# Kernel tuning notes

Hardware: AMD Instinct MI355X
Metric: run time of the kernel (lower is better)

The kernel has to match this reference:

```python
import jax, jax.numpy as jnp
import numpy as np

K = 3          # kernel_size
STRIDE = 1
PAD = 1
DIL = 1


def setup_inputs() -> dict:
    key = jax.random.key(0)
    k1, k2, k3, k4, k5 = jax.random.split(key, 5)
    x = jax.random.normal(k1, (4, 64, 128, 128), jnp.float32)
    weight = jax.random.normal(k2, (64, 64, K, K), jnp.float32) * 0.05   # [O, C, K, K]
    bias = jax.random.normal(k3, (64,), jnp.float32) * 0.05
    # offset conv params: small nonzero so offsets actually exercise bilinear sampling
    offset_w = jax.random.normal(k4, (2 * K * K, 64, K, K), jnp.float32) * 0.01
    offset_b = jax.random.normal(k5, (2 * K * K,), jnp.float32) * 0.1
    return {"x": x, "weight": weight, "bias": bias,
            "offset_w": offset_w, "offset_b": offset_b}


def _conv2d(x, w, b):
    y = jax.lax.conv_general_dilated(
        x, w, window_strides=(STRIDE, STRIDE),
        padding=((PAD, PAD), (PAD, PAD)), rhs_dilation=(DIL, DIL),
        dimension_numbers=("NCHW", "OIHW", "NCHW"))
    return y + b[None, :, None, None]


def _bilinear_sample(img, ys, xs):
    # img: [C, H, W]; ys, xs: [KK, Ho, Wo] float sampling coords
    H, W = img.shape[1], img.shape[2]
    y0 = jnp.floor(ys)
    x0 = jnp.floor(xs)
    y1 = y0 + 1.0
    x1 = x0 + 1.0
    wy1 = ys - y0
    wx1 = xs - x0
    wy0 = 1.0 - wy1
    wx0 = 1.0 - wx1

    def gather(yy, xx):
        valid = (yy >= 0) & (yy <= H - 1) & (xx >= 0) & (xx <= W - 1)
        yi = jnp.clip(yy, 0, H - 1).astype(jnp.int32)
        xi = jnp.clip(xx, 0, W - 1).astype(jnp.int32)
        v = img[:, yi, xi]                     # [C, KK, Ho, Wo]
        return v * valid.astype(img.dtype)

    return (gather(y0, x0) * (wy0 * wx0) + gather(y0, x1) * (wy0 * wx1)
            + gather(y1, x0) * (wy1 * wx0) + gather(y1, x1) * (wy1 * wx1))


def reference(x, weight, bias, offset_w, offset_b):
    B, C, H, W = x.shape
    KK = K * K
    # offsets: [B, 2*K*K, Ho, Wo], per-location (dy, dx) for each kernel tap
    offset = _conv2d(x, offset_w, offset_b)
    Ho, Wo = offset.shape[2], offset.shape[3]
    off = offset.reshape(B, KK, 2, Ho, Wo)
    dy, dx = off[:, :, 0], off[:, :, 1]        # [B, KK, Ho, Wo]

    ki, kj = jnp.meshgrid(jnp.arange(K), jnp.arange(K), indexing="ij")
    ki = ki.reshape(KK).astype(x.dtype)
    kj = kj.reshape(KK).astype(x.dtype)
    oy = (jnp.arange(Ho) * STRIDE - PAD).astype(x.dtype)
    ox = (jnp.arange(Wo) * STRIDE - PAD).astype(x.dtype)
    base_y = oy[None, :, None] + (ki * DIL)[:, None, None]   # [KK, Ho, 1]
    base_x = ox[None, None, :] + (kj * DIL)[:, None, None]   # [KK, 1, Wo]
    ys = base_y[None] + dy                                   # [B, KK, Ho, Wo]
    xs = base_x[None] + dx

    # sampled: [B, C, KK, Ho, Wo]
    sampled = jax.vmap(_bilinear_sample)(x, ys, xs)
    w = weight.reshape(weight.shape[0], C, KK)
    out = jnp.einsum("bckhw,ock->bohw", sampled, w) + bias[None, :, None, None]
    return out
```

## Files before the change

kernel.cpp:

```cpp
#include <hip/hip_runtime.h>
#include <hip/hip_bf16.h>

#define B_ 4
#define C_ 64
#define H_ 128
#define W_ 128
#define HW_ (H_ * W_)
#define OCH_ 18

typedef __attribute__((ext_vector_type(8))) short short8;
typedef __attribute__((ext_vector_type(16))) float f32x16;

#define W2B_ELEMS (9 * 2 * 4 * 64 * 8)
#define W2A_ELEMS (36 * 64 * 8)
#define OFF_BYTE_OFS 131072
#define XH_BYTE_OFS  2490368
#define WS_NEED (XH_BYTE_OFS + (size_t)B_ * H_ * W_ * C_ * 2)

#define PSTRIDE_B 10256
#define WIN_BYTES (4 * PSTRIDE_B)

__device__ __forceinline__ unsigned short f2bf(float f) {
  union { float f; unsigned u; } v; v.f = f;
  unsigned r = v.u + 0x7FFFu + ((v.u >> 16) & 1u);
  return (unsigned short)(r >> 16);
}
__device__ __forceinline__ float bf2f(unsigned short h) {
  union { unsigned u; float f; } v; v.u = ((unsigned)h) << 16;
  return v.f;
}
__device__ __forceinline__ short f2bfh(float f) {
  __hip_bfloat16 h = __float2bfloat16(f);
  return *reinterpret_cast<short*>(&h);
}
__device__ __forceinline__ int swz512(int x) { return (x & 7) * 64 + (x >> 3); }

__device__ __forceinline__ void pack_weights_body(
    int idx, const float* __restrict__ wmain, const float* __restrict__ offw,
    unsigned short* __restrict__ ws_u) {
  if (idx < W2B_ELEMS) {
    int i = idx & 7, lane = (idx >> 3) & 63, s = (idx >> 9) & 3;
    int mq = (idx >> 11) & 1, t = idx >> 12;
    int o = mq * 32 + (lane & 31);
    int c = 16 * s + (lane >> 5) * 8 + i;
    ws_u[idx] = f2bf(wmain[(o * 64 + c) * 9 + t]);
  } else if (idx < W2B_ELEMS + W2A_ELEMS) {
    int j = idx - W2B_ELEMS;
    int i = j & 7, lane = (j >> 3) & 63, s = j >> 9;
    int kg = 16 * s + (lane >> 5) * 8 + i;
    int t = kg >> 6, c = kg & 63, oc = lane & 31;
    ws_u[idx] = (oc < OCH_) ? f2bf(offw[(oc * 64 + c) * 9 + t]) : (unsigned short)0;
  }
}

__global__ __launch_bounds__(256) void prep_kernel(
    const float* __restrict__ x, const float* __restrict__ wmain,
    const float* __restrict__ offw, unsigned short* __restrict__ ws_u,
    unsigned short* __restrict__ xh) {
  const int tid = threadIdx.x;
  if (blockIdx.x < 512) {
    __shared__ float s[W_ * 65];
    const int h = blockIdx.x & (H_ - 1);
    const int b = blockIdx.x >> 7;
    const float* xb = x + ((size_t)b * C_ * H_ + h) * W_;
    for (int i = tid; i < C_ * W_; i += 256) {
      int c = i >> 7, w = i & (W_ - 1);
      s[w * 65 + c] = xb[(size_t)c * HW_ + w];
    }
    __syncthreads();
    unsigned short* dst = xh + ((size_t)(b * H_ + h) * W_) * C_;
    for (int i = tid; i < W_ * 8; i += 256) {
      int w = i >> 3, g = i & 7;
      short8 v;
      #pragma unroll
      for (int j = 0; j < 8; ++j) v[j] = (short)f2bf(s[w * 65 + g * 8 + j]);
      *(short8*)&dst[w * C_ + g * 8] = v;
    }
  } else {
    pack_weights_body((blockIdx.x - 512) * 256 + tid, wmain, offw, ws_u);
  }
}

__global__ __launch_bounds__(256) void pack_w_only(
    const float* __restrict__ wmain, const float* __restrict__ offw,
    unsigned short* __restrict__ ws_u) {
  pack_weights_body(blockIdx.x * 256 + threadIdx.x, wmain, offw, ws_u);
}

template<int KI, int KJ, int CPH>
__device__ __forceinline__ void tap_body(
    float dy, float dx, int ho, int px, int lane, int b,
    const char* __restrict__ win, const unsigned short* __restrict__ xh,
    const unsigned short* __restrict__ wt2,
    f32x16& acc0, f32x16& acc1) {
  const float ys = (float)(ho - 1 + KI) + dy;
  const float xs = (float)(px - 1 + KJ) + dx;
  const float y0f = floorf(ys), x0f = floorf(xs);
  const int y0 = (int)y0f, x0 = (int)x0f;
  const int y1 = y0 + 1, x1 = x0 + 1;
  const float wy1 = ys - y0f, wx1 = xs - x0f;
  const float wy0 = 1.f - wy1, wx0 = 1.f - wx1;
  const bool vy0 = (unsigned)y0 < (unsigned)H_, vy1 = (unsigned)y1 < (unsigned)H_;
  const bool vx0 = (unsigned)x0 < (unsigned)W_, vx1 = (unsigned)x1 < (unsigned)W_;
  const float g00 = (vy0 && vx0) ? wy0 * wx0 : 0.f;
  const float g01 = (vy0 && vx1) ? wy0 * wx1 : 0.f;
  const float g10 = (vy1 && vx0) ? wy1 * wx0 : 0.f;
  const float g11 = (vy1 && vx1) ? wy1 * wx1 : 0.f;
  const int yc0 = min(max(y0, 0), H_ - 1), yc1 = min(max(y1, 0), H_ - 1);
  const int xc0 = min(max(x0, 0), W_ - 1), xc1 = min(max(x1, 0), W_ - 1);
  const int rr0 = yc0 - ho + 2, rr1 = yc1 - ho + 2;
  const bool in0 = (unsigned)rr0 < 5u, in1 = (unsigned)rr1 < 5u;
  const int r0 = min(max(rr0, 0), 4), r1 = min(max(rr1, 0), 4);
  const int u00 = (r0 * 128 + xc0) << 4, u01 = (r0 * 128 + xc1) << 4;
  const int u10 = (r1 * 128 + xc0) << 4, u11 = (r1 * 128 + xc1) << 4;
  const int laneh = lane >> 5;
  #pragma unroll
  for (int ssl = 0; ssl < 2; ++ssl) {
    const int ss = CPH * 2 + ssl;
    const char* pb = win + (2 * ssl + laneh) * PSTRIDE_B;
    short8 c00 = *(const short8*)(pb + u00);
    short8 c01 = *(const short8*)(pb + u01);
    short8 c10 = *(const short8*)(pb + u10);
    short8 c11 = *(const short8*)(pb + u11);
    if (!in0 || !in1) {
      const int ch8 = (2 * ss + laneh) << 3;
      if (!in0) {
        c00 = *(const short8*)&xh[(((size_t)((b * H_ + yc0) * W_ + xc0)) << 6) + ch8];
        c01 = *(const short8*)&xh[(((size_t)((b * H_ + yc0) * W_ + xc1)) << 6) + ch8];
      }
      if (!in1) {
        c10 = *(const short8*)&xh[(((size_t)((b * H_ + yc1) * W_ + xc0)) << 6) + ch8];
        c11 = *(const short8*)&xh[(((size_t)((b * H_ + yc1) * W_ + xc1)) << 6) + ch8];
      }
    }
    short8 bf;
    #pragma unroll
    for (int i = 0; i < 8; ++i) {
      float v = g00 * bf2f((unsigned short)c00[i]) + g01 * bf2f((unsigned short)c01[i])
              + g10 * bf2f((unsigned short)c10[i]) + g11 * bf2f((unsigned short)c11[i]);
      bf[i] = f2bfh(v);
    }
    const short8 a0 = *(const short8*)&wt2[(ss * 64 + lane) * 8];
    const short8 a1 = *(const short8*)&wt2[((4 + ss) * 64 + lane) * 8];
    acc0 = __builtin_amdgcn_mfma_f32_32x32x16_bf16(a0, bf, acc0, 0, 0, 0);
    acc1 = __builtin_amdgcn_mfma_f32_32x32x16_bf16(a1, bf, acc1, 0, 0, 0);
  }
}

#define STAGEW(CPH)                                                                     \
  _Pragma("unroll")                                                                     \
  for (int it = 0; it < 5; ++it) {                                                      \
    const int i = tid + it * 512;                                                       \
    const int p = i & 3;                                                                \
    const int xcol = (i >> 2) & 127;                                                    \
    const int r = i >> 9;                                                               \
    const int srow = min(H_ - 1, max(0, ho - 2 + r));                                   \
    const short8 v = *(const short8*)&xh[(((size_t)((b * H_ + srow) * W_ + xcol)) << 6) \
                                         + ((4 * (CPH) + p) << 3)];                     \
    *(short8*)(smem + p * PSTRIDE_B + ((r * 128 + xcol) << 4)) = v;                     \
  }

#define P1HALF(CPH)                                                                     \
  _Pragma("unroll")                                                                     \
  for (int t = 0; t < 9; ++t) {                                                         \
    _Pragma("unroll")                                                                   \
    for (int q = 0; q < 2; ++q) {                                                       \
      const int s = 4 * t + 2 * (CPH) + q;                                              \
      const int ki = t / 3, kj = t - 3 * (t / 3);                                       \
      const int row = ho - 1 + ki, col = px - 1 + kj;                                   \
      short8 bfr = {0, 0, 0, 0, 0, 0, 0, 0};                                            \
      if (((unsigned)row < (unsigned)H_) && ((unsigned)col < (unsigned)W_))             \
        bfr = *(const short8*)(smem + (2 * q + laneh) * PSTRIDE_B                       \
                               + (((ki + 1) * 128 + col) << 4));                        \
      const short8 afr = *(const short8*)&w2a[((size_t)s * 64 + lane) * 8];             \
      pacc = __builtin_amdgcn_mfma_f32_32x32x16_bf16(afr, bfr, pacc, 0, 0, 0);          \
    }                                                                                   \
  }

#define EXT(T, J)                                                                       \
  {                                                                                     \
    constexpr int ocy = 2 * (T), ocx = 2 * (T) + 1;                                     \
    constexpr int ry = (ocy & 3) + 4 * (ocy >> 3), hy = (ocy >> 2) & 1;                 \
    constexpr int rx = (ocx & 3) + 4 * (ocx >> 3), hx = (ocx >> 2) & 1;                 \
    dys[J] = __shfl(pacc[ry], (lane & 31) + (hy << 5)) + ob[ocy];                       \
    dxs[J] = __shfl(pacc[rx], (lane & 31) + (hx << 5)) + ob[ocx];                       \
  }

#define TAP(KI, KJ, CPH, J)                                                             \
  tap_body<KI, KJ, CPH>(dys[J], dxs[J], ho, px, lane, b, smem, xh,                      \
                        w2b + ((KI) * 3 + (KJ)) * 4096, acc0, acc1)

#define P2CPH(CPH)                                                                      \
  if (sub == 0) {                                                                       \
    TAP(0, 0, CPH, 0); TAP(0, 1, CPH, 1); TAP(0, 2, CPH, 2); TAP(1, 0, CPH, 3);         \
  } else {                                                                              \
    TAP(1, 1, CPH, 0); TAP(1, 2, CPH, 1); TAP(2, 0, CPH, 2); TAP(2, 1, CPH, 3);         \
    TAP(2, 2, CPH, 4);                                                                  \
  }

__global__ __launch_bounds__(512, 4) void deform_fused2(
    const unsigned short* __restrict__ xh, const float* __restrict__ bias,
    const float* __restrict__ ob, const unsigned short* __restrict__ w2b,
    const unsigned short* __restrict__ w2a, float* __restrict__ out) {
  const int blk = swz512(blockIdx.x);
  const int ho = blk & (H_ - 1);
  const int b  = blk >> 7;
  const int tid = threadIdx.x;
  const int lane = tid & 63;
  const int wave = tid >> 6;
  const int pair = wave >> 1;
  const int sub  = wave & 1;
  const int px   = pair * 32 + (lane & 31);
  const int laneh = lane >> 5;

  __shared__ __align__(16) char smem[WIN_BYTES];

  f32x16 pacc;
  #pragma unroll
  for (int r = 0; r < 16; ++r) pacc[r] = 0.f;

  STAGEW(0);
  __syncthreads();
  P1HALF(0);
  __syncthreads();
  STAGEW(1);
  __syncthreads();
  P1HALF(1);

  float dys[5], dxs[5];
  if (sub == 0) {
    EXT(0, 0); EXT(1, 1); EXT(2, 2); EXT(3, 3);
    dys[4] = 0.f; dxs[4] = 0.f;
  } else {
    EXT(4, 0); EXT(5, 1); EXT(6, 2); EXT(7, 3); EXT(8, 4);
  }

  f32x16 acc0, acc1;
  #pragma unroll
  for (int r = 0; r < 16; ++r) { acc0[r] = 0.f; acc1[r] = 0.f; }

  P2CPH(1);
  __syncthreads();
  STAGEW(0);
  __syncthreads();
  P2CPH(0);
  __syncthreads();

  float* red = (float*)smem;
  if (sub) {
    #pragma unroll
    for (int i = 0; i < 16; ++i) {
      red[(i * 4 + pair) * 64 + lane]        = acc0[i];
      red[((16 + i) * 4 + pair) * 64 + lane] = acc1[i];
    }
  }
  __syncthreads();
  if (!sub) {
    #pragma unroll
    for (int i = 0; i < 16; ++i) {
      acc0[i] += red[(i * 4 + pair) * 64 + lane];
      acc1[i] += red[((16 + i) * 4 + pair) * 64 + lane];
    }
    #pragma unroll
    for (int reg = 0; reg < 16; ++reg) {
      int row = (reg & 3) + 8 * (reg >> 2) + 4 * laneh;
      out[((b * 64 + row)      * H_ + ho) * W_ + px] = acc0[reg] + bias[row];
      out[((b * 64 + 32 + row) * H_ + ho) * W_ + px] = acc1[reg] + bias[32 + row];
    }
  }
}

__global__ __launch_bounds__(256) void offset_conv_mfma(
    const float* __restrict__ x, const float* __restrict__ ob,
    const unsigned short* __restrict__ w2a, unsigned short* __restrict__ offout) {
  const int ho = blockIdx.x & (H_ - 1);
  const int b  = blockIdx.x >> 7;
  const int tid = threadIdx.x;
  const int lane = tid & 63;
  const int wv = tid >> 6;
  __shared__ __align__(16) unsigned short sx[3 * 130 * 64];
  const float* xb = x + (size_t)b * C_ * HW_;
  for (int i = tid; i < 96 * 130; i += 256) {
    int col = i % 130;
    int c2  = i / 130;
    int r   = c2 >> 5;
    int c   = (c2 & 31) * 2;
    int row = ho - 1 + r, gcol = col - 1;
    float v0 = 0.f, v1 = 0.f;
    if ((unsigned)row < (unsigned)H_ && (unsigned)gcol < (unsigned)W_) {
      v0 = xb[(size_t)c * HW_ + row * W_ + gcol];
      v1 = xb[(size_t)(c + 1) * HW_ + row * W_ + gcol];
    }
    unsigned pk = (unsigned)f2bf(v0) | ((unsigned)f2bf(v1) << 16);
    int cblk = (c >> 3) ^ (col & 7);
    int h = ((r * 130 + col) * 8 + cblk) * 8 + (c & 7);
    *(unsigned*)&sx[h] = pk;
  }
  __syncthreads();
  const int px  = wv * 32 + (lane & 31);
  const int cbh = lane >> 5;
  f32x16 acc;
  #pragma unroll
  for (int r = 0; r < 16; ++r) acc[r] = 0.f;
  for (int s = 0; s < 36; ++s) {
    int t  = s >> 2;
    int ki = t / 3, kj = t - 3 * ki;
    int j  = px + kj;
    int cblk = (s & 3) * 2 + cbh;
    const short8 bfr = *(const short8*)&sx[((ki * 130 + j) * 8 + (cblk ^ (j & 7))) * 8];
    const short8 afr = *(const short8*)&w2a[(s * 64 + lane) * 8];
    acc = __builtin_amdgcn_mfma_f32_32x32x16_bf16(afr, bfr, acc, 0, 0, 0);
  }
  #pragma unroll
  for (int reg = 0; reg < 16; ++reg) {
    int oc = (reg & 3) + 8 * (reg >> 2) + 4 * (lane >> 5);
    if (oc < OCH_) {
      float v = acc[reg] + ob[oc];
      offout[((b * OCH_ + oc) * H_ + ho) * W_ + px] = f2bf(v);
    }
  }
}

__global__ __launch_bounds__(256) void deform_mfma(
    const float* __restrict__ x, const float* __restrict__ bias,
    const unsigned short* __restrict__ w2b, const unsigned short* __restrict__ offb,
    float* __restrict__ out) {
  const int ho = blockIdx.x & (H_ - 1);
  const int b  = blockIdx.x >> 7;
  const int lane = threadIdx.x & 63;
  const int wv   = threadIdx.x >> 6;
  const int px   = wv * 32 + (lane & 31);
  const int cb   = (lane >> 5) * 8;
  const float* xb = x + (size_t)b * C_ * HW_;
  f32x16 acc0, acc1;
  #pragma unroll
  for (int r = 0; r < 16; ++r) { acc0[r] = 0.f; acc1[r] = 0.f; }
  for (int t = 0; t < 9; ++t) {
    const int ki = t / 3, kj = t - 3 * ki;
    float dy = bf2f(offb[((b * OCH_ + 2 * t)     * H_ + ho) * W_ + px]);
    float dx = bf2f(offb[((b * OCH_ + 2 * t + 1) * H_ + ho) * W_ + px]);
    float ys = (float)(ho - 1 + ki) + dy;
    float xs = (float)(px - 1 + kj) + dx;
    float y0f = floorf(ys), x0f = floorf(xs);
    int y0 = (int)y0f, x0 = (int)x0f;
    int y1 = y0 + 1,   x1 = x0 + 1;
    float wy1 = ys - y0f, wx1 = xs - x0f;
    float wy0 = 1.f - wy1, wx0 = 1.f - wx1;
    bool vy0 = (unsigned)y0 < (unsigned)H_, vy1 = (unsigned)y1 < (unsigned)H_;
    bool vx0 = (unsigned)x0 < (unsigned)W_, vx1 = (unsigned)x1 < (unsigned)W_;
    int yc0 = min(max(y0, 0), H_ - 1), yc1 = min(max(y1, 0), H_ - 1);
    int xc0 = min(max(x0, 0), W_ - 1), xc1 = min(max(x1, 0), W_ - 1);
    const int o00 = yc0 * W_ + xc0, o01 = yc0 * W_ + xc1;
    const int o10 = yc1 * W_ + xc0, o11 = yc1 * W_ + xc1;
    const float g00 = (vy0 && vx0) ? wy0 * wx0 : 0.f;
    const float g01 = (vy0 && vx1) ? wy0 * wx1 : 0.f;
    const float g10 = (vy1 && vx0) ? wy1 * wx0 : 0.f;
    const float g11 = (vy1 && vx1) ? wy1 * wx1 : 0.f;
    const short8* wp = (const short8*)(w2b + (size_t)t * 2 * 4 * 64 * 8);
    short8 a0[4], a1[4];
    #pragma unroll
    for (int s = 0; s < 4; ++s) {
      a0[s] = wp[s * 64 + lane];
      a1[s] = wp[(4 + s) * 64 + lane];
    }
    #pragma unroll
    for (int s = 0; s < 4; ++s) {
      const int cidx = (cb + 16 * s) * HW_;
      short8 bf;
      #pragma unroll
      for (int i = 0; i < 8; ++i) {
        const int bi = cidx + i * HW_;
        float v = g00 * xb[bi + o00] + g01 * xb[bi + o01]
                + g10 * xb[bi + o10] + g11 * xb[bi + o11];
        bf[i] = (short)f2bf(v);
      }
      acc0 = __builtin_amdgcn_mfma_f32_32x32x16_bf16(a0[s], bf, acc0, 0, 0, 0);
      acc1 = __builtin_amdgcn_mfma_f32_32x32x16_bf16(a1[s], bf, acc1, 0, 0, 0);
    }
  }
  #pragma unroll
  for (int reg = 0; reg < 16; ++reg) {
    int row = (reg & 3) + 8 * (reg >> 2) + 4 * (lane >> 5);
    out[((b * 64 + row)      * H_ + ho) * W_ + px] = acc0[reg] + bias[row];
    out[((b * 64 + 32 + row) * H_ + ho) * W_ + px] = acc1[reg] + bias[32 + row];
  }
}

extern "C" void kernel_launch(void* const* d_in, const int* in_sizes, int n_in,
                              void* d_out, int out_size, void* d_ws, size_t ws_size,
                              hipStream_t stream) {
  const float* x    = (const float*)d_in[0];
  const float* wt   = (const float*)d_in[1];
  const float* bias = (const float*)d_in[2];
  const float* ow   = (const float*)d_in[3];
  const float* ob   = (const float*)d_in[4];
  float* out = (float*)d_out;

  unsigned short* ws_u  = (unsigned short*)d_ws;
  unsigned short* w2b   = ws_u;
  unsigned short* w2a   = ws_u + W2B_ELEMS;
  unsigned short* offbf = (unsigned short*)((char*)d_ws + OFF_BYTE_OFS);
  unsigned short* xh    = (unsigned short*)((char*)d_ws + XH_BYTE_OFS);

  const int pack_blocks = (W2B_ELEMS + W2A_ELEMS + 255) / 256;

  if (ws_size >= WS_NEED) {
    prep_kernel<<<512 + pack_blocks, 256, 0, stream>>>(x, wt, ow, ws_u, xh);
    deform_fused2<<<512, 512, 0, stream>>>(xh, bias, ob, w2b, w2a, out);
  } else {
    pack_w_only<<<pack_blocks, 256, 0, stream>>>(wt, ow, ws_u);
    offset_conv_mfma<<<B_ * H_, 256, 0, stream>>>(x, ob, w2a, offbf);
    deform_mfma<<<B_ * H_, 256, 0, stream>>>(x, bias, w2b, offbf, out);
  }
}
```

Measured before the change: 43.05 us.

## Split fused deformable conv into half-row tiles with narrower LDS window

The fused kernel now processes half an output row (64 columns) per block with 256 threads instead of a full row with 512, doubling the grid to 1024 blocks. The staged LDS window shrinks to 72 columns with halo, which lowers shared memory per block and may raise occupancy. Samples falling outside the window fall back to global loads. The bilinear blend also unpacks bf16 pairs with packed float2 arithmetic. In exchange, neighbouring blocks restage overlapping halo columns, and more samples take the slower global-memory path.

Result: slower. 45.94 us (+6.7%).

```diff
diff --git a/kernel.cpp b/kernel.cpp
--- a/kernel.cpp
+++ b/kernel.cpp
@@ -10,6 +10,7 @@
 
 typedef __attribute__((ext_vector_type(8))) short short8;
 typedef __attribute__((ext_vector_type(16))) float f32x16;
+typedef __attribute__((ext_vector_type(2))) float float2v;
 
 #define W2B_ELEMS (9 * 2 * 4 * 64 * 8)
 #define W2A_ELEMS (36 * 64 * 8)
@@ -17,7 +18,8 @@
 #define XH_BYTE_OFS  2490368
 #define WS_NEED (XH_BYTE_OFS + (size_t)B_ * H_ * W_ * C_ * 2)
 
-#define PSTRIDE_B 10256
+#define WCOLS 72
+#define PSTRIDE_B (5 * WCOLS * 16 + 16)
 #define WIN_BYTES (4 * PSTRIDE_B)
 
 __device__ __forceinline__ unsigned short f2bf(float f) {
@@ -29,11 +31,15 @@
   union { unsigned u; float f; } v; v.u = ((unsigned)h) << 16;
   return v.f;
 }
-__device__ __forceinline__ short f2bfh(float f) {
+__device__ __forceinline__ unsigned short f2bfh(float f) {
   __hip_bfloat16 h = __float2bfloat16(f);
-  return *reinterpret_cast<short*>(&h);
-}
-__device__ __forceinline__ int swz512(int x) { return (x & 7) * 64 + (x >> 3); }
+  return *reinterpret_cast<unsigned short*>(&h);
+}
+__device__ __forceinline__ float uaf(unsigned u) {
+  union { unsigned u; float f; } v; v.u = u; return v.f;
+}
+__device__ __forceinline__ int swz512(int x)  { return (x & 7) * 64  + (x >> 3); }
+__device__ __forceinline__ int swz1024(int x) { return (x & 7) * 128 + (x >> 3); }
 
 __device__ __forceinline__ void pack_weights_body(
     int idx, const float* __restrict__ wmain, const float* __restrict__ offw,
@@ -89,7 +95,7 @@
 
 template<int KI, int KJ, int CPH>
 __device__ __forceinline__ void tap_body(
-    float dy, float dx, int ho, int px, int lane, int b,
+    float dy, float dx, int ho, int wo0, int px, int lane, int b,
     const char* __restrict__ win, const unsigned short* __restrict__ xh,
     const unsigned short* __restrict__ wt2,
     f32x16& acc0, f32x16& acc1) {
@@ -109,10 +115,13 @@
   const int yc0 = min(max(y0, 0), H_ - 1), yc1 = min(max(y1, 0), H_ - 1);
   const int xc0 = min(max(x0, 0), W_ - 1), xc1 = min(max(x1, 0), W_ - 1);
   const int rr0 = yc0 - ho + 2, rr1 = yc1 - ho + 2;
-  const bool in0 = (unsigned)rr0 < 5u, in1 = (unsigned)rr1 < 5u;
+  const int cc0 = xc0 - wo0 + 4, cc1 = xc1 - wo0 + 4;
+  const bool inw = ((unsigned)rr0 < 5u) & ((unsigned)rr1 < 5u) &
+                   ((unsigned)cc0 < (unsigned)WCOLS) & ((unsigned)cc1 < (unsigned)WCOLS);
   const int r0 = min(max(rr0, 0), 4), r1 = min(max(rr1, 0), 4);
-  const int u00 = (r0 * 128 + xc0) << 4, u01 = (r0 * 128 + xc1) << 4;
-  const int u10 = (r1 * 128 + xc0) << 4, u11 = (r1 * 128 + xc1) << 4;
+  const int c0 = min(max(cc0, 0), WCOLS - 1), c1 = min(max(cc1, 0), WCOLS - 1);
+  const int u00 = (r0 * WCOLS + c0) << 4, u01 = (r0 * WCOLS + c1) << 4;
+  const int u10 = (r1 * WCOLS + c0) << 4, u11 = (r1 * WCOLS + c1) << 4;
   const int laneh = lane >> 5;
   #pragma unroll
   for (int ssl = 0; ssl < 2; ++ssl) {
@@ -122,23 +131,27 @@
     short8 c01 = *(const short8*)(pb + u01);
     short8 c10 = *(const short8*)(pb + u10);
     short8 c11 = *(const short8*)(pb + u11);
-    if (!in0 || !in1) {
-      const int ch8 = (2 * ss + laneh) << 3;
-      if (!in0) {
-        c00 = *(const short8*)&xh[(((size_t)((b * H_ + yc0) * W_ + xc0)) << 6) + ch8];
-        c01 = *(const short8*)&xh[(((size_t)((b * H_ + yc0) * W_ + xc1)) << 6) + ch8];
-      }
-      if (!in1) {
-        c10 = *(const short8*)&xh[(((size_t)((b * H_ + yc1) * W_ + xc0)) << 6) + ch8];
-        c11 = *(const short8*)&xh[(((size_t)((b * H_ + yc1) * W_ + xc1)) << 6) + ch8];
-      }
+    if (!inw) {
+      const size_t ch8 = (size_t)((2 * ss + laneh) << 3);
+      c00 = *(const short8*)&xh[(((size_t)((b * H_ + yc0) * W_ + xc0)) << 6) + ch8];
+      c01 = *(const short8*)&xh[(((size_t)((b * H_ + yc0) * W_ + xc1)) << 6) + ch8];
+      c10 = *(const short8*)&xh[(((size_t)((b * H_ + yc1) * W_ + xc0)) << 6) + ch8];
+      c11 = *(const short8*)&xh[(((size_t)((b * H_ + yc1) * W_ + xc1)) << 6) + ch8];
     }
     short8 bf;
     #pragma unroll
-    for (int i = 0; i < 8; ++i) {
-      float v = g00 * bf2f((unsigned short)c00[i]) + g01 * bf2f((unsigned short)c01[i])
-              + g10 * bf2f((unsigned short)c10[i]) + g11 * bf2f((unsigned short)c11[i]);
-      bf[i] = f2bfh(v);
+    for (int d = 0; d < 4; ++d) {
+      const unsigned w00 = ((const unsigned*)&c00)[d];
+      const unsigned w01 = ((const unsigned*)&c01)[d];
+      const unsigned w10 = ((const unsigned*)&c10)[d];
+      const unsigned w11 = ((const unsigned*)&c11)[d];
+      float2v p00, p01, p10, p11;
+      p00.x = uaf(w00 << 16); p00.y = uaf(w00 & 0xFFFF0000u);
+      p01.x = uaf(w01 << 16); p01.y = uaf(w01 & 0xFFFF0000u);
+      p10.x = uaf(w10 << 16); p10.y = uaf(w10 & 0xFFFF0000u);
+      p11.x = uaf(w11 << 16); p11.y = uaf(w11 & 0xFFFF0000u);
+      float2v v = p00 * g00 + p01 * g01 + p10 * g10 + p11 * g11;
+      ((unsigned*)&bf)[d] = (unsigned)f2bfh(v.x) | ((unsigned)f2bfh(v.y) << 16);
     }
     const short8 a0 = *(const short8*)&wt2[(ss * 64 + lane) * 8];
     const short8 a1 = *(const short8*)&wt2[((4 + ss) * 64 + lane) * 8];
@@ -147,17 +160,23 @@
   }
 }
 
+#define NLOAD (4 * 5 * WCOLS)
+
 #define STAGEW(CPH)                                                                     \
   _Pragma("unroll")                                                                     \
-  for (int it = 0; it < 5; ++it) {                                                      \
-    const int i = tid + it * 512;                                                       \
-    const int p = i & 3;                                                                \
-    const int xcol = (i >> 2) & 127;                                                    \
-    const int r = i >> 9;                                                               \
-    const int srow = min(H_ - 1, max(0, ho - 2 + r));                                   \
-    const short8 v = *(const short8*)&xh[(((size_t)((b * H_ + srow) * W_ + xcol)) << 6) \
-                                         + ((4 * (CPH) + p) << 3)];                     \
-    *(short8*)(smem + p * PSTRIDE_B + ((r * 128 + xcol) << 4)) = v;                     \
+  for (int it = 0; it < 6; ++it) {                                                      \
+    const int i = tid + it * 256;                                                       \
+    if (i < NLOAD) {                                                                    \
+      const int p = i & 3;                                                              \
+      const int j = i >> 2;                                                             \
+      const int col = j % WCOLS;                                                        \
+      const int r = j / WCOLS;                                                          \
+      const int srow = min(H_ - 1, max(0, ho - 2 + r));                                 \
+      const int scol = min(W_ - 1, max(0, wo0 - 4 + col));                              \
+      const short8 v = *(const short8*)&xh[(((size_t)((b * H_ + srow) * W_ + scol)) << 6) \
+                                           + ((4 * (CPH) + p) << 3)];                   \
+      *(short8*)(smem + p * PSTRIDE_B + ((r * WCOLS + col) << 4)) = v;                  \
+    }                                                                                   \
   }
 
 #define P1HALF(CPH)                                                                     \
@@ -171,7 +190,7 @@
       short8 bfr = {0, 0, 0, 0, 0, 0, 0, 0};                                            \
       if (((unsigned)row < (unsigned)H_) && ((unsigned)col < (unsigned)W_))             \
         bfr = *(const short8*)(smem + (2 * q + laneh) * PSTRIDE_B                       \
-                               + (((ki + 1) * 128 + col) << 4));                        \
+                               + (((ki + 1) * WCOLS + (pxl + 3 + kj)) << 4));           \
       const short8 afr = *(const short8*)&w2a[((size_t)s * 64 + lane) * 8];             \
       pacc = __builtin_amdgcn_mfma_f32_32x32x16_bf16(afr, bfr, pacc, 0, 0, 0);          \
     }                                                                                   \
@@ -187,7 +206,7 @@
   }
 
 #define TAP(KI, KJ, CPH, J)                                                             \
-  tap_body<KI, KJ, CPH>(dys[J], dxs[J], ho, px, lane, b, smem, xh,                      \
+  tap_body<KI, KJ, CPH>(dys[J], dxs[J], ho, wo0, px, lane, b, smem, xh,                 \
                         w2b + ((KI) * 3 + (KJ)) * 4096, acc0, acc1)
 
 #define P2CPH(CPH)                                                                      \
@@ -198,19 +217,22 @@
     TAP(2, 2, CPH, 4);                                                                  \
   }
 
-__global__ __launch_bounds__(512, 4) void deform_fused2(
+__global__ __launch_bounds__(256, 4) void deform_fused3(
     const unsigned short* __restrict__ xh, const float* __restrict__ bias,
     const float* __restrict__ ob, const unsigned short* __restrict__ w2b,
     const unsigned short* __restrict__ w2a, float* __restrict__ out) {
-  const int blk = swz512(blockIdx.x);
-  const int ho = blk & (H_ - 1);
-  const int b  = blk >> 7;
+  const int blk = swz1024(blockIdx.x);
+  const int whalf = blk & 1;
+  const int ho = (blk >> 1) & (H_ - 1);
+  const int b  = blk >> 8;
+  const int wo0 = whalf * 64;
   const int tid = threadIdx.x;
   const int lane = tid & 63;
   const int wave = tid >> 6;
   const int pair = wave >> 1;
   const int sub  = wave & 1;
-  const int px   = pair * 32 + (lane & 31);
+  const int pxl  = pair * 32 + (lane & 31);
+  const int px   = wo0 + pxl;
   const int laneh = lane >> 5;
 
   __shared__ __align__(16) char smem[WIN_BYTES];
@@ -250,16 +272,16 @@
   if (sub) {
     #pragma unroll
     for (int i = 0; i < 16; ++i) {
-      red[(i * 4 + pair) * 64 + lane]        = acc0[i];
-      red[((16 + i) * 4 + pair) * 64 + lane] = acc1[i];
+      red[(i * 2 + pair) * 64 + lane]        = acc0[i];
+      red[((16 + i) * 2 + pair) * 64 + lane] = acc1[i];
     }
   }
   __syncthreads();
   if (!sub) {
     #pragma unroll
     for (int i = 0; i < 16; ++i) {
-      acc0[i] += red[(i * 4 + pair) * 64 + lane];
-      acc1[i] += red[((16 + i) * 4 + pair) * 64 + lane];
+      acc0[i] += red[(i * 2 + pair) * 64 + lane];
+      acc1[i] += red[((16 + i) * 2 + pair) * 64 + lane];
     }
     #pragma unroll
     for (int reg = 0; reg < 16; ++reg) {
@@ -406,7 +428,7 @@
 
   if (ws_size >= WS_NEED) {
     prep_kernel<<<512 + pack_blocks, 256, 0, stream>>>(x, wt, ow, ws_u, xh);
-    deform_fused2<<<512, 512, 0, stream>>>(xh, bias, ob, w2b, w2a, out);
+    deform_fused3<<<1024, 256, 0, stream>>>(xh, bias, ob, w2b, w2a, out);
   } else {
     pack_w_only<<<pack_blocks, 256, 0, stream>>>(wt, ow, ws_u);
     offset_conv_mfma<<<B_ * H_, 256, 0, stream>>>(x, ob, w2a, offbf);
```

## Prefetch staged windows into registers to overlap global loads with MFMA phases

Applied to the files above, without the earlier changes.

Splits the shared-memory window staging into a register-prefetch issue step and a later write step, so global loads for the next channel half (and for the phase-2 restage) are in flight while the offset-conv MFMAs run. It also splits the offset accumulator into two independent MFMA chains to break the serial dependency, and vectorises the prep kernel's transpose loads to float4. The cost is extra registers (five short8 staging values plus a second accumulator) under a 512-thread, 4-block launch bound, which may cause spills or lower occupancy.

After: 44.82 us. 4.1% more time.

```diff
diff --git a/kernel.cpp b/kernel.cpp
--- a/kernel.cpp
+++ b/kernel.cpp
@@ -63,9 +63,13 @@
     const int h = blockIdx.x & (H_ - 1);
     const int b = blockIdx.x >> 7;
     const float* xb = x + ((size_t)b * C_ * H_ + h) * W_;
-    for (int i = tid; i < C_ * W_; i += 256) {
-      int c = i >> 7, w = i & (W_ - 1);
-      s[w * 65 + c] = xb[(size_t)c * HW_ + w];
+    for (int i = tid; i < C_ * W_ / 4; i += 256) {
+      int c = i >> 5, q = i & 31;
+      float4 v = *reinterpret_cast<const float4*>(&xb[(size_t)c * HW_ + q * 4]);
+      s[(q * 4 + 0) * 65 + c] = v.x;
+      s[(q * 4 + 1) * 65 + c] = v.y;
+      s[(q * 4 + 2) * 65 + c] = v.z;
+      s[(q * 4 + 3) * 65 + c] = v.w;
     }
     __syncthreads();
     unsigned short* dst = xh + ((size_t)(b * H_ + h) * W_) * C_;
@@ -147,17 +151,28 @@
   }
 }
 
-#define STAGEW(CPH)                                                                     \
+#define STAGE_ISSUE(CPH)                                                                \
   _Pragma("unroll")                                                                     \
   for (int it = 0; it < 5; ++it) {                                                      \
     const int i = tid + it * 512;                                                       \
     const int p = i & 3;                                                                \
-    const int xcol = (i >> 2) & 127;                                                    \
-    const int r = i >> 9;                                                               \
+    const int j = i >> 2;                                                               \
+    const int col = j & 127;                                                            \
+    const int r = j >> 7;                                                               \
     const int srow = min(H_ - 1, max(0, ho - 2 + r));                                   \
-    const short8 v = *(const short8*)&xh[(((size_t)((b * H_ + srow) * W_ + xcol)) << 6) \
-                                         + ((4 * (CPH) + p) << 3)];                     \
-    *(short8*)(smem + p * PSTRIDE_B + ((r * 128 + xcol) << 4)) = v;                     \
+    stg[it] = *(const short8*)&xh[(((size_t)((b * H_ + srow) * W_ + col)) << 6)         \
+                                  + ((4 * (CPH) + p) << 3)];                            \
+  }
+
+#define STAGE_WRITE()                                                                   \
+  _Pragma("unroll")                                                                     \
+  for (int it = 0; it < 5; ++it) {                                                      \
+    const int i = tid + it * 512;                                                       \
+    const int p = i & 3;                                                                \
+    const int j = i >> 2;                                                               \
+    const int col = j & 127;                                                            \
+    const int r = j >> 7;                                                               \
+    *(short8*)(smem + p * PSTRIDE_B + ((r * 128 + col) << 4)) = stg[it];                \
   }
 
 #define P1HALF(CPH)                                                                     \
@@ -173,7 +188,10 @@
         bfr = *(const short8*)(smem + (2 * q + laneh) * PSTRIDE_B                       \
                                + (((ki + 1) * 128 + col) << 4));                        \
       const short8 afr = *(const short8*)&w2a[((size_t)s * 64 + lane) * 8];             \
-      pacc = __builtin_amdgcn_mfma_f32_32x32x16_bf16(afr, bfr, pacc, 0, 0, 0);          \
+      if (q == 0)                                                                       \
+        pacc_a = __builtin_amdgcn_mfma_f32_32x32x16_bf16(afr, bfr, pacc_a, 0, 0, 0);    \
+      else                                                                              \
+        pacc_b = __builtin_amdgcn_mfma_f32_32x32x16_bf16(afr, bfr, pacc_b, 0, 0, 0);    \
     }                                                                                   \
   }
 
@@ -198,7 +216,7 @@
     TAP(2, 2, CPH, 4);                                                                  \
   }
 
-__global__ __launch_bounds__(512, 4) void deform_fused2(
+__global__ __launch_bounds__(512, 4) void deform_fused4(
     const unsigned short* __restrict__ xh, const float* __restrict__ bias,
     const float* __restrict__ ob, const unsigned short* __restrict__ w2b,
     const unsigned short* __restrict__ w2a, float* __restrict__ out) {
@@ -215,17 +233,28 @@
 
   __shared__ __align__(16) char smem[WIN_BYTES];
 
+  short8 stg[5];
+
+  f32x16 pacc_a, pacc_b;
+  #pragma unroll
+  for (int r = 0; r < 16; ++r) { pacc_a[r] = 0.f; pacc_b[r] = 0.f; }
+
+  STAGE_ISSUE(0);
+  STAGE_WRITE();
+  __syncthreads();
+
+  STAGE_ISSUE(1);
+  P1HALF(0);
+  __syncthreads();
+  STAGE_WRITE();
+  __syncthreads();
+
+  STAGE_ISSUE(0);
+  P1HALF(1);
+
   f32x16 pacc;
   #pragma unroll
-  for (int r = 0; r < 16; ++r) pacc[r] = 0.f;
-
-  STAGEW(0);
-  __syncthreads();
-  P1HALF(0);
-  __syncthreads();
-  STAGEW(1);
-  __syncthreads();
-  P1HALF(1);
+  for (int r = 0; r < 16; ++r) pacc[r] = pacc_a[r] + pacc_b[r];
 
   float dys[5], dxs[5];
   if (sub == 0) {
@@ -241,7 +270,7 @@
 
   P2CPH(1);
   __syncthreads();
-  STAGEW(0);
+  STAGE_WRITE();
   __syncthreads();
   P2CPH(0);
   __syncthreads();
@@ -406,7 +435,7 @@
 
   if (ws_size >= WS_NEED) {
     prep_kernel<<<512 + pack_blocks, 256, 0, stream>>>(x, wt, ow, ws_u, xh);
-    deform_fused2<<<512, 512, 0, stream>>>(xh, bias, ob, w2b, w2a, out);
+    deform_fused4<<<512, 512, 0, stream>>>(xh, bias, ob, w2b, w2a, out);
   } else {
     pack_w_only<<<pack_blocks, 256, 0, stream>>>(wt, ow, ws_u);
     offset_conv_mfma<<<B_ * H_, 256, 0, stream>>>(x, ob, w2a, offbf);
```

## Stage full 64-channel window once and split offset conv across wave pairs

Applied to the files above, without the earlier changes.

The fused deformable-conv kernel now stages all 64 channels of the 5-row input window into shared memory in a single pass, using register-batched loads, instead of two half-channel passes that needed restaging and extra barriers. The offset-conv MFMA work is split between the two waves of each pair, each doing half the k-steps with two independent accumulators. Their partial sums are reduced through shared memory rather than by shuffles. The prep kernel transposes input with float4 loads. Shared memory roughly doubles and launch bounds drop to 2 blocks per CU, which may reduce occupancy.

Result: no change. 42.43 us (-1.4%).

```diff
diff --git a/kernel.cpp b/kernel.cpp
--- a/kernel.cpp
+++ b/kernel.cpp
@@ -18,7 +18,9 @@
 #define WS_NEED (XH_BYTE_OFS + (size_t)B_ * H_ * W_ * C_ * 2)
 
 #define PSTRIDE_B 10256
-#define WIN_BYTES (4 * PSTRIDE_B)
+#define WIN_BYTES (8 * PSTRIDE_B)
+#define PART_OFS  WIN_BYTES
+#define SMEM_BYTES (WIN_BYTES + 2 * 4 * 18 * 32 * 4)
 
 __device__ __forceinline__ unsigned short f2bf(float f) {
   union { float f; unsigned u; } v; v.f = f;
@@ -63,9 +65,13 @@
     const int h = blockIdx.x & (H_ - 1);
     const int b = blockIdx.x >> 7;
     const float* xb = x + ((size_t)b * C_ * H_ + h) * W_;
-    for (int i = tid; i < C_ * W_; i += 256) {
-      int c = i >> 7, w = i & (W_ - 1);
-      s[w * 65 + c] = xb[(size_t)c * HW_ + w];
+    for (int i = tid; i < C_ * W_ / 4; i += 256) {
+      int c = i >> 5, q = i & 31;
+      float4 v = *reinterpret_cast<const float4*>(&xb[(size_t)c * HW_ + q * 4]);
+      s[(q * 4 + 0) * 65 + c] = v.x;
+      s[(q * 4 + 1) * 65 + c] = v.y;
+      s[(q * 4 + 2) * 65 + c] = v.z;
+      s[(q * 4 + 3) * 65 + c] = v.w;
     }
     __syncthreads();
     unsigned short* dst = xh + ((size_t)(b * H_ + h) * W_) * C_;
@@ -87,8 +93,8 @@
   pack_weights_body(blockIdx.x * 256 + threadIdx.x, wmain, offw, ws_u);
 }
 
-template<int KI, int KJ, int CPH>
-__device__ __forceinline__ void tap_body(
+template<int KI, int KJ>
+__device__ __forceinline__ void tap_full(
     float dy, float dx, int ho, int px, int lane, int b,
     const char* __restrict__ win, const unsigned short* __restrict__ xh,
     const unsigned short* __restrict__ wt2,
@@ -115,9 +121,8 @@
   const int u10 = (r1 * 128 + xc0) << 4, u11 = (r1 * 128 + xc1) << 4;
   const int laneh = lane >> 5;
   #pragma unroll
-  for (int ssl = 0; ssl < 2; ++ssl) {
-    const int ss = CPH * 2 + ssl;
-    const char* pb = win + (2 * ssl + laneh) * PSTRIDE_B;
+  for (int ss = 0; ss < 4; ++ss) {
+    const char* pb = win + (2 * ss + laneh) * PSTRIDE_B;
     short8 c00 = *(const short8*)(pb + u00);
     short8 c01 = *(const short8*)(pb + u01);
     short8 c10 = *(const short8*)(pb + u10);
@@ -147,58 +152,11 @@
   }
 }
 
-#define STAGEW(CPH)                                                                     \
-  _Pragma("unroll")                                                                     \
-  for (int it = 0; it < 5; ++it) {                                                      \
-    const int i = tid + it * 512;                                                       \
-    const int p = i & 3;                                                                \
-    const int xcol = (i >> 2) & 127;                                                    \
-    const int r = i >> 9;                                                               \
-    const int srow = min(H_ - 1, max(0, ho - 2 + r));                                   \
-    const short8 v = *(const short8*)&xh[(((size_t)((b * H_ + srow) * W_ + xcol)) << 6) \
-                                         + ((4 * (CPH) + p) << 3)];                     \
-    *(short8*)(smem + p * PSTRIDE_B + ((r * 128 + xcol) << 4)) = v;                     \
-  }
-
-#define P1HALF(CPH)                                                                     \
-  _Pragma("unroll")                                                                     \
-  for (int t = 0; t < 9; ++t) {                                                         \
-    _Pragma("unroll")                                                                   \
-    for (int q = 0; q < 2; ++q) {                                                       \
-      const int s = 4 * t + 2 * (CPH) + q;                                              \
-      const int ki = t / 3, kj = t - 3 * (t / 3);                                       \
-      const int row = ho - 1 + ki, col = px - 1 + kj;                                   \
-      short8 bfr = {0, 0, 0, 0, 0, 0, 0, 0};                                            \
-      if (((unsigned)row < (unsigned)H_) && ((unsigned)col < (unsigned)W_))             \
-        bfr = *(const short8*)(smem + (2 * q + laneh) * PSTRIDE_B                       \
-                               + (((ki + 1) * 128 + col) << 4));                        \
-      const short8 afr = *(const short8*)&w2a[((size_t)s * 64 + lane) * 8];             \
-      pacc = __builtin_amdgcn_mfma_f32_32x32x16_bf16(afr, bfr, pacc, 0, 0, 0);          \
-    }                                                                                   \
-  }
-
-#define EXT(T, J)                                                                       \
-  {                                                                                     \
-    constexpr int ocy = 2 * (T), ocx = 2 * (T) + 1;                                     \
-    constexpr int ry = (ocy & 3) + 4 * (ocy >> 3), hy = (ocy >> 2) & 1;                 \
-    constexpr int rx = (ocx & 3) + 4 * (ocx >> 3), hx = (ocx >> 2) & 1;                 \
-    dys[J] = __shfl(pacc[ry], (lane & 31) + (hy << 5)) + ob[ocy];                       \
-    dxs[J] = __shfl(pacc[rx], (lane & 31) + (hx << 5)) + ob[ocx];                       \
-  }
-
-#define TAP(KI, KJ, CPH, J)                                                             \
-  tap_body<KI, KJ, CPH>(dys[J], dxs[J], ho, px, lane, b, smem, xh,                      \
-                        w2b + ((KI) * 3 + (KJ)) * 4096, acc0, acc1)
-
-#define P2CPH(CPH)                                                                      \
-  if (sub == 0) {                                                                       \
-    TAP(0, 0, CPH, 0); TAP(0, 1, CPH, 1); TAP(0, 2, CPH, 2); TAP(1, 0, CPH, 3);         \
-  } else {                                                                              \
-    TAP(1, 1, CPH, 0); TAP(1, 2, CPH, 1); TAP(2, 0, CPH, 2); TAP(2, 1, CPH, 3);         \
-    TAP(2, 2, CPH, 4);                                                                  \
-  }
-
-__global__ __launch_bounds__(512, 4) void deform_fused2(
+#define TAP(KI, KJ, J)                                                                  \
+  tap_full<KI, KJ>(dys[J], dxs[J], ho, px, lane, b, smem, xh,                           \
+                   w2b + ((KI) * 3 + (KJ)) * 4096, acc0, acc1)
+
+__global__ __launch_bounds__(512, 2) void deform_fused5(
     const unsigned short* __restrict__ xh, const float* __restrict__ bias,
     const float* __restrict__ ob, const unsigned short* __restrict__ w2b,
     const unsigned short* __restrict__ w2a, float* __restrict__ out) {
@@ -211,39 +169,90 @@
   const int pair = wave >> 1;
   const int sub  = wave & 1;
   const int px   = pair * 32 + (lane & 31);
+  const int pxl  = lane & 31;
   const int laneh = lane >> 5;
 
-  __shared__ __align__(16) char smem[WIN_BYTES];
-
-  f32x16 pacc;
-  #pragma unroll
-  for (int r = 0; r < 16; ++r) pacc[r] = 0.f;
-
-  STAGEW(0);
+  __shared__ __align__(16) char smem[SMEM_BYTES];
+
+  short8 stg[10];
+  #pragma unroll
+  for (int it = 0; it < 10; ++it) {
+    const int i = tid + it * 512;
+    const int p = i & 7;
+    const int col = (i >> 3) & 127;
+    const int r = i >> 10;
+    const int srow = min(H_ - 1, max(0, ho - 2 + r));
+    stg[it] = *(const short8*)&xh[(((size_t)((b * H_ + srow) * W_ + col)) << 6) + (p << 3)];
+  }
+  #pragma unroll
+  for (int it = 0; it < 10; ++it) {
+    const int i = tid + it * 512;
+    const int p = i & 7;
+    const int col = (i >> 3) & 127;
+    const int r = i >> 10;
+    *(short8*)(smem + p * PSTRIDE_B + ((r * 128 + col) << 4)) = stg[it];
+  }
   __syncthreads();
-  P1HALF(0);
+
+  f32x16 pacc_a, pacc_b;
+  #pragma unroll
+  for (int r = 0; r < 16; ++r) { pacc_a[r] = 0.f; pacc_b[r] = 0.f; }
+
+  const int s0 = sub * 18;
+  #pragma unroll
+  for (int q = 0; q < 18; ++q) {
+    const int s  = s0 + q;
+    const int t  = s >> 2;
+    const int ki = t / 3, kj = t - 3 * (t / 3);
+    const int row = ho - 1 + ki;
+    const int col = px - 1 + kj;
+    short8 bfr = {0, 0, 0, 0, 0, 0, 0, 0};
+    if (((unsigned)row < (unsigned)H_) && ((unsigned)col < (unsigned)W_))
+      bfr = *(const short8*)(smem + ((s & 3) * 2 + laneh) * PSTRIDE_B
+                             + (((ki + 1) * 128 + col) << 4));
+    const short8 afr = *(const short8*)&w2a[((size_t)s * 64 + lane) * 8];
+    if (q & 1)
+      pacc_b = __builtin_amdgcn_mfma_f32_32x32x16_bf16(afr, bfr, pacc_b, 0, 0, 0);
+    else
+      pacc_a = __builtin_amdgcn_mfma_f32_32x32x16_bf16(afr, bfr, pacc_a, 0, 0, 0);
+  }
+
+  {
+    float* part = (float*)(smem + PART_OFS);
+    #pragma unroll
+    for (int reg = 0; reg < 16; ++reg) {
+      const int oc = (reg & 3) + 8 * (reg >> 2) + 4 * laneh;
+      if (oc < OCH_)
+        part[(((pair << 1) + sub) * OCH_ + oc) * 32 + pxl] = pacc_a[reg] + pacc_b[reg];
+    }
+  }
   __syncthreads();
-  STAGEW(1);
-  __syncthreads();
-  P1HALF(1);
-
+
+  const int t0 = sub * 4;
+  const int nt = 4 + sub;
   float dys[5], dxs[5];
+  {
+    const float* part = (const float*)(smem + PART_OFS);
+    const int base0 = ((pair << 1) + 0) * OCH_ * 32 + pxl;
+    const int base1 = ((pair << 1) + 1) * OCH_ * 32 + pxl;
+    #pragma unroll
+    for (int j = 0; j < 5; ++j) {
+      int tt = t0 + ((j < nt) ? j : 0);
+      int ocy = 2 * tt, ocx = 2 * tt + 1;
+      dys[j] = part[base0 + ocy * 32] + part[base1 + ocy * 32] + ob[ocy];
+      dxs[j] = part[base0 + ocx * 32] + part[base1 + ocx * 32] + ob[ocx];
+    }
+  }
+
+  f32x16 acc0, acc1;
+  #pragma unroll
+  for (int r = 0; r < 16; ++r) { acc0[r] = 0.f; acc1[r] = 0.f; }
+
   if (sub == 0) {
-    EXT(0, 0); EXT(1, 1); EXT(2, 2); EXT(3, 3);
-    dys[4] = 0.f; dxs[4] = 0.f;
+    TAP(0, 0, 0); TAP(0, 1, 1); TAP(0, 2, 2); TAP(1, 0, 3);
   } else {
-    EXT(4, 0); EXT(5, 1); EXT(6, 2); EXT(7, 3); EXT(8, 4);
-  }
-
-  f32x16 acc0, acc1;
-  #pragma unroll
-  for (int r = 0; r < 16; ++r) { acc0[r] = 0.f; acc1[r] = 0.f; }
-
-  P2CPH(1);
-  __syncthreads();
-  STAGEW(0);
-  __syncthreads();
-  P2CPH(0);
+    TAP(1, 1, 0); TAP(1, 2, 1); TAP(2, 0, 2); TAP(2, 1, 3); TAP(2, 2, 4);
+  }
   __syncthreads();
 
   float* red = (float*)smem;
@@ -406,7 +415,7 @@
 
   if (ws_size >= WS_NEED) {
     prep_kernel<<<512 + pack_blocks, 256, 0, stream>>>(x, wt, ow, ws_u, xh);
-    deform_fused2<<<512, 512, 0, stream>>>(xh, bias, ob, w2b, w2a, out);
+    deform_fused5<<<512, 512, 0, stream>>>(xh, bias, ob, w2b, w2a, out);
   } else {
     pack_w_only<<<pack_blocks, 256, 0, stream>>>(wt, ow, ws_u);
     offset_conv_mfma<<<B_ * H_, 256, 0, stream>>>(x, ob, w2a, offbf);
```
